# Kernel optimization log

Hardware: AMD Instinct MI355X
Metric: run time of the kernel (lower is better)

## Reference

```python
import jax, jax.numpy as jnp
import numpy as np

N_NODES = 50000
N_EDGES = 800000
IN_DIM = 128
HID = 64
OUT_DIM = 128
N_GRAPHS = 128


def setup_inputs() -> dict:
    key = jax.random.key(0)
    ks = jax.random.split(key, 16)

    def lin(k, fan_in, fan_out):
        k1, k2 = jax.random.split(k)
        bound = 1.0 / np.sqrt(fan_in)
        W = jax.random.uniform(k1, (fan_in, fan_out), jnp.float32, -bound, bound)
        b = jax.random.uniform(k2, (fan_out,), jnp.float32, -bound, bound)
        return W, b

    x = jax.random.normal(ks[0], (N_NODES, IN_DIM), jnp.float32)
    edge_index = jax.random.randint(ks[1], (2, N_EDGES), 0, N_NODES, jnp.int64)
    batch = jnp.sort(jax.random.randint(ks[2], (N_NODES,), 0, N_GRAPHS, jnp.int64))

    W_in, b_in = lin(ks[3], IN_DIM, HID)
    W1_0, b1_0 = lin(ks[4], HID, HID)
    W2_0, b2_0 = lin(ks[5], HID, HID)
    W1_1, b1_1 = lin(ks[6], HID, HID)
    W2_1, b2_1 = lin(ks[7], HID, HID)
    W_out, b_out = lin(ks[8], HID, OUT_DIM)

    return dict(x=x, edge_index=edge_index, batch=batch,
                W_in=W_in, b_in=b_in,
                W1_0=W1_0, b1_0=b1_0, W2_0=W2_0, b2_0=b2_0,
                W1_1=W1_1, b1_1=b1_1, W2_1=W2_1, b2_1=b2_1,
                W_out=W_out, b_out=b_out)


def _gin_conv(x, src, dst, W1, b1, W2, b2):
    # aggr[i] = sum_{(s,i) in E} x[s]; GIN (eps=0): h = MLP(x + aggr)
    msgs = x[src]  # [E, HID] gather
    aggr = jax.ops.segment_sum(msgs, dst, num_segments=N_NODES)
    h = x + aggr
    h = jax.nn.relu(h @ W1 + b1)
    return h @ W2 + b2


def reference(x, edge_index, batch,
              W_in, b_in,
              W1_0, b1_0, W2_0, b2_0,
              W1_1, b1_1, W2_1, b2_1,
              W_out, b_out):
    src, dst = edge_index[0], edge_index[1]
    h = x @ W_in + b_in  # proj_in
    # conv 0 (+ReLU; dropout is identity in eval mode)
    h = jax.nn.relu(_gin_conv(h, src, dst, W1_0, b1_0, W2_0, b2_0))
    # conv 1
    h = jax.nn.relu(_gin_conv(h, src, dst, W1_1, b1_1, W2_1, b2_1))
    h = h @ W_out + b_out  # proj_out -> [N, OUT_DIM]
    # global mean pool over graphs
    sums = jax.ops.segment_sum(h, batch, num_segments=N_GRAPHS)
    counts = jax.ops.segment_sum(jnp.ones((h.shape[0],), h.dtype), batch, num_segments=N_GRAPHS)
    graph_emb = sums / jnp.maximum(counts, 1.0)[:, None]  # [N_GRAPHS, OUT_DIM]
    return graph_emb
```

## Files before the change

kernel.cpp:

```cpp
#include <hip/hip_runtime.h>
#include <hip/hip_fp16.h>

#define N_NODES   50000
#define N_EDGES   800000
#define IN_DIM    128
#define HID       64
#define OUT_DIM   128
#define N_GRAPHS  128

#define NBKT      196
#define BBLK      392
#define BSTRIDE   5120
#define CAP       42
#define SRCSTRIDE 10240

#define OFF_GCUR   0
#define OFF_GSUM   196
#define OFF_GSTART 8388
#define OFF_ROWPTR 8518
#define OFF_EPAIRS 458520
#define OFF_HA     1462040
#define OFF_HB     2262056
#define OFF_WT     3062072

typedef float v2f __attribute__((ext_vector_type(2)));
typedef float f32x4 __attribute__((ext_vector_type(4)));
typedef short bf16x8 __attribute__((ext_vector_type(8)));

union FragU { uint4 u; bf16x8 v; };

__device__ __forceinline__ unsigned short f2bf(float f) {
    union { float f; unsigned int u; } v; v.f = f;
    const unsigned int r = v.u + 0x7FFFu + ((v.u >> 16) & 1u);
    return (unsigned short)(r >> 16);
}

__device__ __forceinline__ void acc_fp8x8(float acc[8], const uint2 w) {
    const v2f a = __builtin_amdgcn_cvt_pk_f32_fp8(w.x, false);
    const v2f b = __builtin_amdgcn_cvt_pk_f32_fp8(w.x, true);
    const v2f c = __builtin_amdgcn_cvt_pk_f32_fp8(w.y, false);
    const v2f d = __builtin_amdgcn_cvt_pk_f32_fp8(w.y, true);
    acc[0] += a.x; acc[1] += a.y; acc[2] += b.x; acc[3] += b.y;
    acc[4] += c.x; acc[5] += c.y; acc[6] += d.x; acc[7] += d.y;
}

__device__ __forceinline__ uint2 pack_fp8x8(const float f[8]) {
    int w0 = 0, w1 = 0;
    w0 = __builtin_amdgcn_cvt_pk_fp8_f32(f[0], f[1], w0, false);
    w0 = __builtin_amdgcn_cvt_pk_fp8_f32(f[2], f[3], w0, true);
    w1 = __builtin_amdgcn_cvt_pk_fp8_f32(f[4], f[5], w1, false);
    w1 = __builtin_amdgcn_cvt_pk_fp8_f32(f[6], f[7], w1, true);
    uint2 r; r.x = (unsigned)w0; r.y = (unsigned)w1;
    return r;
}

#define K1_SMEM_BYTES 34816

__device__ __forceinline__ void role_bucket(char* smem, const int* __restrict__ ei,
                                            int* __restrict__ gcur,
                                            unsigned int* __restrict__ epairs,
                                            int bid) {
    int* lcnt = (int*)smem;
    unsigned int* stage = (unsigned int*)(smem + NBKT * 4);
    const int t = threadIdx.x;
    for (int i = t; i < NBKT; i += 256) lcnt[i] = 0;
    __syncthreads();
    for (int e0 = bid * 512; e0 < N_EDGES; e0 += BBLK * 512) {
#pragma unroll
        for (int half = 0; half < 2; ++half) {
            const int e = e0 + half * 256 + t;
            if (e < N_EDGES) {
                const unsigned int src = (unsigned int)ei[e];
                const unsigned int dst = (unsigned int)ei[N_EDGES + e];
                const int b = dst >> 8;
                const unsigned int pk = src | (dst << 16);
                const int pos = atomicAdd(&lcnt[b], 1);
                if (pos < CAP) stage[b * CAP + pos] = pk;
                else {
                    const int gp = atomicAdd(&gcur[b], 1);
                    epairs[b * BSTRIDE + gp] = pk;
                }
            }
        }
    }
    __syncthreads();
    if (t < NBKT) {
        int n = lcnt[t]; if (n > CAP) n = CAP;
        if (n > 0) {
            const int base = atomicAdd(&gcur[t], n);
            for (int i = 0; i < n; ++i)
                epairs[t * BSTRIDE + base + i] = stage[t * CAP + i];
        }
    }
}

__device__ __forceinline__ void role_gbound(const int* __restrict__ batch,
                                            int* __restrict__ gstart, int bid) {
    const int n = bid * 256 + threadIdx.x;
    if (n >= N_NODES) return;
    const int b = batch[n];
    if (n == 0) {
        for (int g = 0; g <= b; ++g) gstart[g] = 0;
    } else {
        const int p = batch[n - 1];
        for (int g = p + 1; g <= b; ++g) gstart[g] = n;
    }
    if (n == N_NODES - 1) {
        for (int g = b + 1; g <= N_GRAPHS; ++g) gstart[g] = N_NODES;
    }
}

__device__ __forceinline__ void role_wprep(const float* __restrict__ W10,
                                           const float* __restrict__ W20,
                                           const float* __restrict__ W11,
                                           const float* __restrict__ W21,
                                           unsigned short* __restrict__ wtg,
                                           unsigned char* __restrict__ hA,
                                           unsigned char* __restrict__ hB) {
    const int t = threadIdx.x;
    const float* Ws[4] = {W10, W20, W11, W21};
#pragma unroll
    for (int m = 0; m < 4; ++m) {
        unsigned short* o = wtg + 8704 + m * 4608;
        const float* w = Ws[m];
        for (int i = t; i < 64 * 64; i += 256) {
            const int k = i >> 6, c = i & 63;
            o[c * 72 + k] = f2bf(w[i]);
        }
    }
    if (t < 16) {
        ((unsigned int*)(hA + (size_t)N_NODES * HID))[t] = 0u;
        ((unsigned int*)(hB + (size_t)N_NODES * HID))[t] = 0u;
    }
}

__device__ __forceinline__ void role_proj(char* smem, const float* __restrict__ x,
                                          const float* __restrict__ Wi,
                                          const float* __restrict__ b,
                                          unsigned char* __restrict__ h8, int bid) {
    unsigned short* X16 = (unsigned short*)smem;
    unsigned short* Wt  = (unsigned short*)(smem + 17408);
    float* OUT32 = (float*)smem;
    const int t = threadIdx.x;
    const int nb = bid * 64;
    for (int i = t; i < 128 * 64; i += 256) {
        const int k = i >> 6, c = i & 63;
        Wt[c * 136 + k] = f2bf(Wi[i]);
    }
    for (int i = t; i < 64 * (IN_DIM / 4); i += 256) {
        const int n = i >> 5;
        const int k4 = (i & 31) * 4;
        float4 val = make_float4(0.f, 0.f, 0.f, 0.f);
        if (nb + n < N_NODES)
            val = *(const float4*)(x + (size_t)(nb + n) * IN_DIM + k4);
        union { uint2 u; unsigned short s[4]; } pk;
        pk.s[0] = f2bf(val.x); pk.s[1] = f2bf(val.y);
        pk.s[2] = f2bf(val.z); pk.s[3] = f2bf(val.w);
        *(uint2*)&X16[n * 136 + k4] = pk.u;
    }
    __syncthreads();

    const int l = t & 63;
    const int m0 = (t >> 6) * 16;
    const int lrow = l & 15;
    const int lk = (l >> 4) * 8;
    FragU a[4];
#pragma unroll
    for (int s = 0; s < 4; ++s)
        a[s].u = *(const uint4*)&X16[(m0 + lrow) * 136 + s * 32 + lk];
    f32x4 acc[4];
#pragma unroll
    for (int n = 0; n < 4; ++n) {
        const float bv = b[n * 16 + lrow];
        acc[n] = (f32x4){bv, bv, bv, bv};
#pragma unroll
        for (int s = 0; s < 4; ++s) {
            FragU w;
            w.u = *(const uint4*)&Wt[(n * 16 + lrow) * 136 + s * 32 + lk];
            acc[n] = __builtin_amdgcn_mfma_f32_16x16x32_bf16(a[s].v, w.v, acc[n], 0, 0, 0);
        }
    }
    __syncthreads();
#pragma unroll
    for (int n = 0; n < 4; ++n)
#pragma unroll
        for (int r = 0; r < 4; ++r)
            OUT32[(m0 + (l >> 4) * 4 + r) * 68 + n * 16 + lrow] = acc[n][r];
    __syncthreads();
    const int ln = t & 31;
    const int c0 = (t >> 5) * 8;
#pragma unroll
    for (int j = 0; j < 2; ++j) {
        const int n = nb + ln + 32 * j;
        if (n < N_NODES) {
            float f[8];
            const float* src = &OUT32[(ln + 32 * j) * 68 + c0];
            *(float4*)&f[0] = *(const float4*)&src[0];
            *(float4*)&f[4] = *(const float4*)&src[4];
            const uint2 p = pack_fp8x8(f);
            *(uint2*)(h8 + (size_t)n * HID + c0) = p;
        }
    }
}

__global__ __launch_bounds__(256) void k_bg(
        const int* __restrict__ ei, const int* __restrict__ batch,
        int* __restrict__ gcur, unsigned int* __restrict__ epairs,
        int* __restrict__ gstart,
        const float* __restrict__ x, const float* __restrict__ Wi,
        const float* __restrict__ bi, unsigned char* __restrict__ hA,
        unsigned char* __restrict__ hB,
        const float* __restrict__ W10, const float* __restrict__ W20,
        const float* __restrict__ W11, const float* __restrict__ W21,
        unsigned short* __restrict__ wtg) {
    __shared__ __attribute__((aligned(16))) char smem[K1_SMEM_BYTES];
    const int bid = blockIdx.x;
    if (bid < BBLK)              role_bucket(smem, ei, gcur, epairs, bid);
    else if (bid < BBLK + NBKT)  role_gbound(batch, gstart, bid - BBLK);
    else if (bid == BBLK + NBKT) role_wprep(W10, W20, W11, W21, wtg, hA, hB);
    else                         role_proj(smem, x, Wi, bi, hA, bid - (BBLK + NBKT + 1));
}

__global__ __launch_bounds__(256) void k_csr(
        const int* __restrict__ gcur, const unsigned int* __restrict__ epairs,
        int* __restrict__ rowptr2, unsigned short* __restrict__ srclist) {
    __shared__ int lhist[256];
    __shared__ int lcur[256];
    __shared__ int wtot[4];
    __shared__ int lsrc[8192];
    const int b = blockIdx.x;
    const int t = threadIdx.x;
    const int lane = t & 63, wv = t >> 6;
    lhist[t] = 0;
    __syncthreads();
    const int cnt = gcur[b];

    for (int i = t; i < cnt; i += 256)
        atomicAdd(&lhist[(epairs[b * BSTRIDE + i] >> 16) & 255], 1);
    __syncthreads();

    const int d = lhist[t];
    const int p8 = (d + 7) & ~7;
    int incl = p8;
#pragma unroll
    for (int off = 1; off < 64; off <<= 1) {
        const int u = __shfl_up(incl, off, 64);
        if (lane >= off) incl += u;
    }
    if (lane == 63) wtot[wv] = incl;
    __syncthreads();
    int woff = 0;
#pragma unroll
    for (int i = 0; i < 4; ++i) woff += (i < wv) ? wtot[i] : 0;
    const int exclP = woff + incl - p8;
    lcur[t] = exclP;
    const int node = b * 256 + t;
    if (node < N_NODES) rowptr2[node] = (b * SRCSTRIDE + exclP) | ((p8 >> 3) << 24);
    __syncthreads();
    const int padTot = wtot[0] + wtot[1] + wtot[2] + wtot[3];
    for (int i = t; i < padTot; i += 256) lsrc[i] = N_NODES;
    __syncthreads();
    for (int i = t; i < cnt; i += 256) {
        const unsigned int u = epairs[b * BSTRIDE + i];
        const int pos = atomicAdd(&lcur[(u >> 16) & 255], 1);
        lsrc[pos] = (int)(u & 0xFFFFu);
    }
    __syncthreads();
    for (int i = t; i < padTot; i += 256)
        srclist[b * SRCSTRIDE + i] = (unsigned short)lsrc[i];
}

#define S_AB 72

__device__ __forceinline__ void gather8(float acc[8],
                                        const unsigned char* __restrict__ hin8,
                                        const uint4 c, const int q) {
    unsigned s[8] = {c.x & 0xFFFFu, c.x >> 16, c.y & 0xFFFFu, c.y >> 16,
                     c.z & 0xFFFFu, c.z >> 16, c.w & 0xFFFFu, c.w >> 16};
    uint2 r[8];
#pragma unroll
    for (int j = 0; j < 8; ++j)
        r[j] = *(const uint2*)(hin8 + (size_t)s[j] * HID + q * 8);
#pragma unroll
    for (int j = 0; j < 8; ++j) acc_fp8x8(acc, r[j]);
}

template<int POOL>
__global__ __launch_bounds__(256, 4) void k_conv_t(
        const unsigned char* __restrict__ hin8,
        const int* __restrict__ rowptr2, const unsigned short* __restrict__ srclist,
        const unsigned short* __restrict__ W1t_g, const float* __restrict__ b1,
        const unsigned short* __restrict__ W2t_g, const float* __restrict__ b2,
        unsigned char* __restrict__ hout8,
        const int* __restrict__ batch, float* __restrict__ gsum) {
    __shared__ __attribute__((aligned(16))) char csm[36864];
    unsigned short* A16 = (unsigned short*)csm;
    unsigned short* H16 = (unsigned short*)(csm + 9216);
    unsigned short* W1t = (unsigned short*)(csm + 18432);
    unsigned short* W2t = (unsigned short*)(csm + 27648);
    float* OUT32 = (float*)csm;
    const int t = threadIdx.x;
    {
        const uint4* s1 = (const uint4*)W1t_g;
        const uint4* s2 = (const uint4*)W2t_g;
        uint4* d1 = (uint4*)W1t;
        uint4* d2 = (uint4*)W2t;
        for (int i = t; i < 576; i += 256) { d1[i] = s1[i]; d2[i] = s2[i]; }
    }

    const int nb = blockIdx.x * 64;
    const int grp = t >> 3;
    const int q = t & 7;
#pragma unroll
    for (int pass = 0; pass < 2; ++pass) {
        const int nloc = pass * 32 + grp;
        const int node = nb + nloc;
        float acc[8] = {0.f, 0.f, 0.f, 0.f, 0.f, 0.f, 0.f, 0.f};
        if (node < N_NODES) {
            acc_fp8x8(acc, *(const uint2*)(hin8 + (size_t)node * HID + q * 8));
            const int v = rowptr2[node];
            const int beg = v & 0xFFFFFF;
            const int ch = (int)((unsigned)v >> 24);
            if (ch) {
                uint4 idx = *(const uint4*)&srclist[beg];
                for (int i = 0; i < ch; ++i) {
                    const uint4 cur = idx;
                    if (i + 1 < ch) idx = *(const uint4*)&srclist[beg + (i + 1) * 8];
                    gather8(acc, hin8, cur, q);
                }
            }
        }
        union { uint4 u; unsigned short s[8]; } ou;
#pragma unroll
        for (int c = 0; c < 8; ++c) ou.s[c] = f2bf(acc[c]);
        *(uint4*)&A16[nloc * S_AB + q * 8] = ou.u;
    }
    __syncthreads();

    const int l = t & 63;
    const int m0 = (t >> 6) * 16;
    const int lrow = l & 15;
    const int lk = (l >> 4) * 8;

    FragU a0, a1;
    a0.u = *(const uint4*)&A16[(m0 + lrow) * S_AB + lk];
    a1.u = *(const uint4*)&A16[(m0 + lrow) * S_AB + 32 + lk];
    f32x4 acc1[4];
#pragma unroll
    for (int n = 0; n < 4; ++n) {
        const float bv = b1[n * 16 + lrow];
        acc1[n] = (f32x4){bv, bv, bv, bv};
        FragU w0, w1;
        w0.u = *(const uint4*)&W1t[(n * 16 + lrow) * S_AB + lk];
        w1.u = *(const uint4*)&W1t[(n * 16 + lrow) * S_AB + 32 + lk];
        acc1[n] = __builtin_amdgcn_mfma_f32_16x16x32_bf16(a0.v, w0.v, acc1[n], 0, 0, 0);
        acc1[n] = __builtin_amdgcn_mfma_f32_16x16x32_bf16(a1.v, w1.v, acc1[n], 0, 0, 0);
    }
    __syncthreads();
#pragma unroll
    for (int n = 0; n < 4; ++n)
#pragma unroll
        for (int r = 0; r < 4; ++r) {
            const int row = m0 + (l >> 4) * 4 + r;
            H16[row * S_AB + n * 16 + lrow] = f2bf(fmaxf(acc1[n][r], 0.0f));
        }
    __syncthreads();

    FragU h0, h1;
    h0.u = *(const uint4*)&H16[(m0 + lrow) * S_AB + lk];
    h1.u = *(const uint4*)&H16[(m0 + lrow) * S_AB + 32 + lk];
    f32x4 acc2[4];
#pragma unroll
    for (int n = 0; n < 4; ++n) {
        const float bv = b2[n * 16 + lrow];
        acc2[n] = (f32x4){bv, bv, bv, bv};
        FragU w0, w1;
        w0.u = *(const uint4*)&W2t[(n * 16 + lrow) * S_AB + lk];
        w1.u = *(const uint4*)&W2t[(n * 16 + lrow) * S_AB + 32 + lk];
        acc2[n] = __builtin_amdgcn_mfma_f32_16x16x32_bf16(h0.v, w0.v, acc2[n], 0, 0, 0);
        acc2[n] = __builtin_amdgcn_mfma_f32_16x16x32_bf16(h1.v, w1.v, acc2[n], 0, 0, 0);
    }
    __syncthreads();
#pragma unroll
    for (int n = 0; n < 4; ++n)
#pragma unroll
        for (int r = 0; r < 4; ++r)
            OUT32[(m0 + (l >> 4) * 4 + r) * 68 + n * 16 + lrow] = fmaxf(acc2[n][r], 0.0f);
    __syncthreads();

    const int ln = t & 31;
    const int c0 = (t >> 5) * 8;
    if constexpr (POOL) {
        const int nlast = (nb + 64 <= N_NODES) ? nb + 63 : N_NODES - 1;
        const int g0 = batch[nb];
        const int g1 = batch[nlast];
        int myg[2];
        float f[2][8];
#pragma unroll
        for (int j = 0; j < 2; ++j) {
            const int n = nb + ln + 32 * j;
            myg[j] = (n < N_NODES) ? batch[n] : -1;
            const float* src = &OUT32[(ln + 32 * j) * 68 + c0];
            *(float4*)&f[j][0] = *(const float4*)&src[0];
            *(float4*)&f[j][4] = *(const float4*)&src[4];
        }
        for (int g = g0; g <= g1; ++g) {
#pragma unroll
            for (int j = 0; j < 2; ++j) {
#pragma unroll
                for (int c = 0; c < 8; ++c) {
                    float v = (myg[j] == g) ? f[j][c] : 0.0f;
#pragma unroll
                    for (int m = 16; m; m >>= 1) v += __shfl_xor(v, m, 64);
                    if (ln == 0) atomicAdd(&gsum[g * HID + c0 + c], v);
                }
            }
        }
    } else {
#pragma unroll
        for (int j = 0; j < 2; ++j) {
            const int n = nb + ln + 32 * j;
            if (n < N_NODES) {
                float f[8];
                const float* src = &OUT32[(ln + 32 * j) * 68 + c0];
                *(float4*)&f[0] = *(const float4*)&src[0];
                *(float4*)&f[4] = *(const float4*)&src[4];
                const uint2 p = pack_fp8x8(f);
                *(uint2*)(hout8 + (size_t)n * HID + c0) = p;
            }
        }
    }
}

__global__ __launch_bounds__(128) void k_out(
        const float* __restrict__ gsum, const int* __restrict__ gstart,
        const float* __restrict__ Wo, const float* __restrict__ bo,
        float* __restrict__ out) {
    __shared__ float mean[HID];
    const int g = blockIdx.x;
    const int t = threadIdx.x;
    const int cnt = gstart[g + 1] - gstart[g];
    if (t < HID)
        mean[t] = (cnt > 0) ? gsum[g * HID + t] / (float)cnt : 0.0f;
    __syncthreads();
    float o = 0.0f;
    for (int k = 0; k < HID; ++k)
        o = fmaf(mean[k], Wo[k * OUT_DIM + t], o);
    out[g * OUT_DIM + t] = (cnt > 0) ? o + bo[t] : 0.0f;
}

extern "C" void kernel_launch(void* const* d_in, const int* in_sizes, int n_in,
                              void* d_out, int out_size, void* d_ws, size_t ws_size,
                              hipStream_t stream) {
    const float* x     = (const float*)d_in[0];
    const int*   ei    = (const int*)d_in[1];
    const int*   batch = (const int*)d_in[2];
    const float* W_in  = (const float*)d_in[3];
    const float* b_in  = (const float*)d_in[4];
    const float* W1_0  = (const float*)d_in[5];
    const float* b1_0  = (const float*)d_in[6];
    const float* W2_0  = (const float*)d_in[7];
    const float* b2_0  = (const float*)d_in[8];
    const float* W1_1  = (const float*)d_in[9];
    const float* b1_1  = (const float*)d_in[10];
    const float* W2_1  = (const float*)d_in[11];
    const float* b2_1  = (const float*)d_in[12];
    const float* W_out = (const float*)d_in[13];
    const float* b_out = (const float*)d_in[14];
    float* out = (float*)d_out;

    unsigned int*   wsw    = (unsigned int*)d_ws;
    int*            gcur   = (int*)(wsw + OFF_GCUR);
    float*          gsum   = (float*)(wsw + OFF_GSUM);
    int*            gstart = (int*)(wsw + OFF_GSTART);
    int*            rowptr = (int*)(wsw + OFF_ROWPTR);
    unsigned int*   epairs = (unsigned int*)(wsw + OFF_EPAIRS);
    unsigned short* srcl   = (unsigned short*)(wsw + OFF_EPAIRS);
    unsigned char*  hA     = (unsigned char*)(wsw + OFF_HA);
    unsigned char*  hB     = (unsigned char*)(wsw + OFF_HB);
    unsigned short* wtg    = (unsigned short*)(wsw + OFF_WT);

    unsigned short* wt10  = wtg + 8704;
    unsigned short* wt20  = wtg + 13312;
    unsigned short* wt11  = wtg + 17920;
    unsigned short* wt21  = wtg + 22528;

    const int pi_blocks = (N_NODES + 63) / 64;
    const int cv_blocks = (N_NODES + 63) / 64;
    const int bg_blocks = BBLK + NBKT + 1 + pi_blocks;

    hipMemsetAsync(gcur, 0, (NBKT + N_GRAPHS * HID) * sizeof(int), stream);
    k_bg<<<bg_blocks, 256, 0, stream>>>(ei, batch, gcur, epairs, gstart,
                                        x, W_in, b_in, hA, hB,
                                        W1_0, W2_0, W1_1, W2_1, wtg);
    k_csr<<<NBKT, 256, 0, stream>>>(gcur, epairs, rowptr, srcl);
    k_conv_t<0><<<cv_blocks, 256, 0, stream>>>(hA, rowptr, srcl,
                                               wt10, b1_0, wt20, b2_0, hB,
                                               batch, gsum);
    k_conv_t<1><<<cv_blocks, 256, 0, stream>>>(hB, rowptr, srcl,
                                               wt11, b1_1, wt21, b2_1, hA,
                                               batch, gsum);
    k_out<<<N_GRAPHS, 128, 0, stream>>>(gsum, gstart, W_out, b_out, out);
}
```

Before: 170.0 us.

## Replace bucketed edge staging with degree-count plus global-cursor scatter CSR build

Replaces the two-stage bucket-then-local-sort CSR construction with a per-node degree count using global atomics, a per-bucket prefix scan that writes row pointers and padding, and a separate scatter kernel that places source ids through per-node atomic cursors. This removes the epairs intermediate buffer and the shared-memory histogram and sort pass. In exchange it adds one kernel launch and two passes of global atomics spread over 50k counters, and neighbor order within a row becomes nondeterministic.

```diff
diff --git a/kernel.cpp b/kernel.cpp
--- a/kernel.cpp
+++ b/kernel.cpp
@@ -9,19 +9,19 @@
 #define N_GRAPHS  128
 
 #define NBKT      196
-#define BBLK      392
-#define BSTRIDE   5120
-#define CAP       42
 #define SRCSTRIDE 10240
-
-#define OFF_GCUR   0
-#define OFF_GSUM   196
-#define OFF_GSTART 8388
-#define OFF_ROWPTR 8518
-#define OFF_EPAIRS 458520
-#define OFF_HA     1462040
-#define OFF_HB     2262056
-#define OFF_WT     3062072
+#define CNTB      391
+#define EPB       2048
+
+#define OFF_GSUM   0
+#define OFF_DEG    8192
+#define OFF_GSTART 58192
+#define OFF_ROWPTR 58324
+#define OFF_CURSOR 108324
+#define OFF_SRCL   158324
+#define OFF_HA     1161844
+#define OFF_HB     1961860
+#define OFF_WT     2761876
 
 typedef float v2f __attribute__((ext_vector_type(2)));
 typedef float f32x4 __attribute__((ext_vector_type(4)));
@@ -56,40 +56,23 @@
 
 #define K1_SMEM_BYTES 34816
 
-__device__ __forceinline__ void role_bucket(char* smem, const int* __restrict__ ei,
-                                            int* __restrict__ gcur,
-                                            unsigned int* __restrict__ epairs,
-                                            int bid) {
-    int* lcnt = (int*)smem;
-    unsigned int* stage = (unsigned int*)(smem + NBKT * 4);
-    const int t = threadIdx.x;
-    for (int i = t; i < NBKT; i += 256) lcnt[i] = 0;
-    __syncthreads();
-    for (int e0 = bid * 512; e0 < N_EDGES; e0 += BBLK * 512) {
-#pragma unroll
-        for (int half = 0; half < 2; ++half) {
-            const int e = e0 + half * 256 + t;
-            if (e < N_EDGES) {
-                const unsigned int src = (unsigned int)ei[e];
-                const unsigned int dst = (unsigned int)ei[N_EDGES + e];
-                const int b = dst >> 8;
-                const unsigned int pk = src | (dst << 16);
-                const int pos = atomicAdd(&lcnt[b], 1);
-                if (pos < CAP) stage[b * CAP + pos] = pk;
-                else {
-                    const int gp = atomicAdd(&gcur[b], 1);
-                    epairs[b * BSTRIDE + gp] = pk;
-                }
-            }
-        }
-    }
-    __syncthreads();
-    if (t < NBKT) {
-        int n = lcnt[t]; if (n > CAP) n = CAP;
-        if (n > 0) {
-            const int base = atomicAdd(&gcur[t], n);
-            for (int i = 0; i < n; ++i)
-                epairs[t * BSTRIDE + base + i] = stage[t * CAP + i];
+__device__ __forceinline__ void role_count(const int* __restrict__ ei,
+                                           int* __restrict__ deg, int bid) {
+    const int t = threadIdx.x;
+    const int base = bid * EPB;
+#pragma unroll
+    for (int off = 0; off < EPB; off += 1024) {
+        const int e = base + off + t * 4;
+        if (e + 4 <= N_EDGES) {
+            const int4 d4 = *(const int4*)&ei[N_EDGES + e];
+            atomicAdd(&deg[d4.x], 1);
+            atomicAdd(&deg[d4.y], 1);
+            atomicAdd(&deg[d4.z], 1);
+            atomicAdd(&deg[d4.w], 1);
+        } else {
+#pragma unroll
+            for (int j = 0; j < 4; ++j)
+                if (e + j < N_EDGES) atomicAdd(&deg[ei[N_EDGES + e + j]], 1);
         }
     }
 }
@@ -203,10 +186,9 @@
     }
 }
 
-__global__ __launch_bounds__(256) void k_bg(
+__global__ __launch_bounds__(256) void k_front(
         const int* __restrict__ ei, const int* __restrict__ batch,
-        int* __restrict__ gcur, unsigned int* __restrict__ epairs,
-        int* __restrict__ gstart,
+        int* __restrict__ deg, int* __restrict__ gstart,
         const float* __restrict__ x, const float* __restrict__ Wi,
         const float* __restrict__ bi, unsigned char* __restrict__ hA,
         unsigned char* __restrict__ hB,
@@ -215,31 +197,21 @@
         unsigned short* __restrict__ wtg) {
     __shared__ __attribute__((aligned(16))) char smem[K1_SMEM_BYTES];
     const int bid = blockIdx.x;
-    if (bid < BBLK)              role_bucket(smem, ei, gcur, epairs, bid);
-    else if (bid < BBLK + NBKT)  role_gbound(batch, gstart, bid - BBLK);
-    else if (bid == BBLK + NBKT) role_wprep(W10, W20, W11, W21, wtg, hA, hB);
-    else                         role_proj(smem, x, Wi, bi, hA, bid - (BBLK + NBKT + 1));
-}
-
-__global__ __launch_bounds__(256) void k_csr(
-        const int* __restrict__ gcur, const unsigned int* __restrict__ epairs,
-        int* __restrict__ rowptr2, unsigned short* __restrict__ srclist) {
-    __shared__ int lhist[256];
-    __shared__ int lcur[256];
+    if (bid < CNTB)              role_count(ei, deg, bid);
+    else if (bid < CNTB + NBKT)  role_gbound(batch, gstart, bid - CNTB);
+    else if (bid == CNTB + NBKT) role_wprep(W10, W20, W11, W21, wtg, hA, hB);
+    else                         role_proj(smem, x, Wi, bi, hA, bid - (CNTB + NBKT + 1));
+}
+
+__global__ __launch_bounds__(256) void k_rows(
+        const int* __restrict__ deg, int* __restrict__ rowptr2,
+        int* __restrict__ cursor, unsigned short* __restrict__ srclist) {
     __shared__ int wtot[4];
-    __shared__ int lsrc[8192];
     const int b = blockIdx.x;
     const int t = threadIdx.x;
     const int lane = t & 63, wv = t >> 6;
-    lhist[t] = 0;
-    __syncthreads();
-    const int cnt = gcur[b];
-
-    for (int i = t; i < cnt; i += 256)
-        atomicAdd(&lhist[(epairs[b * BSTRIDE + i] >> 16) & 255], 1);
-    __syncthreads();
-
-    const int d = lhist[t];
+    const int node = b * 256 + t;
+    const int d = (node < N_NODES) ? deg[node] : 0;
     const int p8 = (d + 7) & ~7;
     int incl = p8;
 #pragma unroll
@@ -252,22 +224,43 @@
     int woff = 0;
 #pragma unroll
     for (int i = 0; i < 4; ++i) woff += (i < wv) ? wtot[i] : 0;
-    const int exclP = woff + incl - p8;
-    lcur[t] = exclP;
-    const int node = b * 256 + t;
-    if (node < N_NODES) rowptr2[node] = (b * SRCSTRIDE + exclP) | ((p8 >> 3) << 24);
-    __syncthreads();
-    const int padTot = wtot[0] + wtot[1] + wtot[2] + wtot[3];
-    for (int i = t; i < padTot; i += 256) lsrc[i] = N_NODES;
-    __syncthreads();
-    for (int i = t; i < cnt; i += 256) {
-        const unsigned int u = epairs[b * BSTRIDE + i];
-        const int pos = atomicAdd(&lcur[(u >> 16) & 255], 1);
-        lsrc[pos] = (int)(u & 0xFFFFu);
-    }
-    __syncthreads();
-    for (int i = t; i < padTot; i += 256)
-        srclist[b * SRCSTRIDE + i] = (unsigned short)lsrc[i];
+    const int pos = b * SRCSTRIDE + woff + incl - p8;
+    if (node < N_NODES) {
+        rowptr2[node] = pos | ((p8 >> 3) << 24);
+        cursor[node]  = pos;
+        for (int i = d; i < p8; ++i)
+            srclist[pos + i] = (unsigned short)N_NODES;
+    }
+}
+
+__global__ __launch_bounds__(256) void k_scat(
+        const int* __restrict__ ei, int* __restrict__ cursor,
+        unsigned short* __restrict__ srclist) {
+    const int t = threadIdx.x;
+    const int base = blockIdx.x * EPB;
+#pragma unroll
+    for (int off = 0; off < EPB; off += 1024) {
+        const int e = base + off + t * 4;
+        if (e + 4 <= N_EDGES) {
+            const int4 s4 = *(const int4*)&ei[e];
+            const int4 d4 = *(const int4*)&ei[N_EDGES + e];
+            const int p0 = atomicAdd(&cursor[d4.x], 1);
+            const int p1 = atomicAdd(&cursor[d4.y], 1);
+            const int p2 = atomicAdd(&cursor[d4.z], 1);
+            const int p3 = atomicAdd(&cursor[d4.w], 1);
+            srclist[p0] = (unsigned short)s4.x;
+            srclist[p1] = (unsigned short)s4.y;
+            srclist[p2] = (unsigned short)s4.z;
+            srclist[p3] = (unsigned short)s4.w;
+        } else {
+#pragma unroll
+            for (int j = 0; j < 4; ++j)
+                if (e + j < N_EDGES) {
+                    const int p = atomicAdd(&cursor[ei[N_EDGES + e + j]], 1);
+                    srclist[p] = (unsigned short)ei[e + j];
+                }
+        }
+    }
 }
 
 #define S_AB 72
@@ -470,12 +463,12 @@
     float* out = (float*)d_out;
 
     unsigned int*   wsw    = (unsigned int*)d_ws;
-    int*            gcur   = (int*)(wsw + OFF_GCUR);
     float*          gsum   = (float*)(wsw + OFF_GSUM);
+    int*            deg    = (int*)(wsw + OFF_DEG);
     int*            gstart = (int*)(wsw + OFF_GSTART);
     int*            rowptr = (int*)(wsw + OFF_ROWPTR);
-    unsigned int*   epairs = (unsigned int*)(wsw + OFF_EPAIRS);
-    unsigned short* srcl   = (unsigned short*)(wsw + OFF_EPAIRS);
+    int*            cursor = (int*)(wsw + OFF_CURSOR);
+    unsigned short* srcl   = (unsigned short*)(wsw + OFF_SRCL);
     unsigned char*  hA     = (unsigned char*)(wsw + OFF_HA);
     unsigned char*  hB     = (unsigned char*)(wsw + OFF_HB);
     unsigned short* wtg    = (unsigned short*)(wsw + OFF_WT);
@@ -487,13 +480,14 @@
 
     const int pi_blocks = (N_NODES + 63) / 64;
     const int cv_blocks = (N_NODES + 63) / 64;
-    const int bg_blocks = BBLK + NBKT + 1 + pi_blocks;
-
-    hipMemsetAsync(gcur, 0, (NBKT + N_GRAPHS * HID) * sizeof(int), stream);
-    k_bg<<<bg_blocks, 256, 0, stream>>>(ei, batch, gcur, epairs, gstart,
-                                        x, W_in, b_in, hA, hB,
-                                        W1_0, W2_0, W1_1, W2_1, wtg);
-    k_csr<<<NBKT, 256, 0, stream>>>(gcur, epairs, rowptr, srcl);
+    const int k1_blocks = CNTB + NBKT + 1 + pi_blocks;
+
+    hipMemsetAsync(gsum, 0, (N_GRAPHS * HID + N_NODES) * sizeof(int), stream);
+    k_front<<<k1_blocks, 256, 0, stream>>>(ei, batch, deg, gstart,
+                                           x, W_in, b_in, hA, hB,
+                                           W1_0, W2_0, W1_1, W2_1, wtg);
+    k_rows<<<NBKT, 256, 0, stream>>>(deg, rowptr, cursor, srcl);
+    k_scat<<<CNTB, 256, 0, stream>>>(ei, cursor, srcl);
     k_conv_t<0><<<cv_blocks, 256, 0, stream>>>(hA, rowptr, srcl,
                                                wt10, b1_0, wt20, b2_0, hB,
                                                batch, gsum);
```

Measured after the change: 224.0 us. 31.8% more time.
